# Kernel optimization log

Measured on AMD Instinct MI355X. Metric: run time of the kernel, lower is better.

The kernel has to match this reference:

```python
import jax, jax.numpy as jnp
import numpy as np

B, LQ, LK = 32, 1024, 1024
Q_SIZE, K_SIZE, HID = 1024, 1024, 1024
NEG = -1e9  # masked_softmax fill value for masked positions


def setup_inputs() -> dict:
    key = jax.random.key(0)
    ks = jax.random.split(key, 8)
    scale_q = 1.0 / np.sqrt(Q_SIZE)
    scale_k = 1.0 / np.sqrt(K_SIZE)
    return {
        "query": jax.random.normal(ks[0], (B, LQ, Q_SIZE), dtype=jnp.float32),
        "key": jax.random.normal(ks[1], (B, LK, K_SIZE), dtype=jnp.float32),
        "query_mask": jax.random.randint(ks[2], (B, LQ), 0, 2, dtype=jnp.int32),
        "key_mask": jax.random.randint(ks[3], (B, LK), 0, 2, dtype=jnp.int32),
        "Wq": jax.random.normal(ks[4], (HID, Q_SIZE), dtype=jnp.float32) * scale_q,
        "bq": jnp.zeros((HID,), dtype=jnp.float32),
        "Wk": jax.random.normal(ks[5], (HID, K_SIZE), dtype=jnp.float32) * scale_k,
        "bk": jnp.zeros((HID,), dtype=jnp.float32),
    }


def reference(query, key, query_mask, key_mask, Wq, bq, Wk, bk):
    # FCNet: weight-norm Linear + ReLU (dropout identity at inference)
    q = jax.nn.relu(jnp.einsum("bqd,hd->bqh", query, Wq) + bq)  # [B,LQ,HID]
    k = jax.nn.relu(jnp.einsum("bkd,hd->bkh", key, Wk) + bk)    # [B,LK,HID]
    logits = jnp.einsum("bqh,bkh->bqk", q, k)                   # [B,LQ,LK]
    # masked_softmax over key dim: masked positions -> -inf
    masked = jnp.where(key_mask[:, None, :] != 0, logits, NEG)
    w = jax.nn.softmax(masked, axis=-1)
    # post-softmax query-mask multiply
    w = w * query_mask.astype(w.dtype)[:, :, None]
    return w
```

## Files before the change

### kernel.cpp

```cpp
#include <hip/hip_runtime.h>
#include <stdint.h>

#define B_SZ 32
#define LQ   1024
#define LK   1024
#define HID  1024
#define KDIM 1024

#define LQC  640
#define NT_M 5

#define BM 128
#define BN 128
#define BK 32

typedef __bf16    bf16x8 __attribute__((ext_vector_type(8)));
typedef _Float16  f16x8  __attribute__((ext_vector_type(8)));
typedef float     f32x4  __attribute__((ext_vector_type(4)));

typedef void __attribute__((address_space(1)))* gptr1_t;
typedef void __attribute__((address_space(3)))* lptr3_t;

__device__ __forceinline__ void async_cp16(const void* g, void* l) {
  __builtin_amdgcn_global_load_lds((gptr1_t)g, (lptr3_t)l, 16, 0, 0);
}

__device__ __forceinline__ __bf16 bits_to_bf16(unsigned short s) {
  return __builtin_bit_cast(__bf16, s);
}

__device__ __forceinline__ void split4(const f32x4 x, bf16x8& hi, bf16x8& lo, int base) {
#pragma unroll
  for (int e = 0; e < 4; ++e) {
    float v = x[e];
    unsigned u = __float_as_uint(v);
    float fh = __uint_as_float(u & 0xffff0000u);
    hi[base + e] = bits_to_bf16((unsigned short)(u >> 16));
    lo[base + e] = (__bf16)(v - fh);
  }
}

__global__ __launch_bounds__(256) void mask_scan2(
    const int* __restrict__ qmask, const int* __restrict__ kmask,
    int* __restrict__ qpos, int* __restrict__ kpos,
    int* __restrict__ qidx, int* __restrict__ kidx,
    int* __restrict__ qcnt, int* __restrict__ kcnt) {
  const int which = blockIdx.x >> 5;
  const int b = blockIdx.x & 31;
  const int* mask = which ? kmask : qmask;
  int* pos = which ? kpos : qpos;
  int* idx = which ? kidx : qidx;
  int* cnt = which ? kcnt : qcnt;

  const int tid = threadIdx.x;
  __shared__ int sums[256];
  int4 m4 = ((const int4*)(mask + b * 1024))[tid];
  int m[4] = {m4.x != 0, m4.y != 0, m4.z != 0, m4.w != 0};
  int local = m[0] + m[1] + m[2] + m[3];
  sums[tid] = local;
  __syncthreads();
  for (int off = 1; off < 256; off <<= 1) {
    int v = (tid >= off) ? sums[tid - off] : 0;
    __syncthreads();
    sums[tid] += v;
    __syncthreads();
  }
  int base = sums[tid] - local;
  int total = sums[255];
  if (total > LQC) total = LQC;
  int p = base;
#pragma unroll
  for (int e = 0; e < 4; ++e) {
    pos[b * 1024 + tid * 4 + e] = p;
    if (m[e] && p < LQC) idx[b * LQC + p] = tid * 4 + e;
    p += m[e];
  }
  if (tid == 0) cnt[b] = total;
  __syncthreads();
  for (int q = total + tid; q < LQC; q += 256) idx[b * LQC + q] = 0;
}

__global__ __launch_bounds__(256) void proj_gemm_c(
    const float* __restrict__ query, const float* __restrict__ key,
    const float* __restrict__ Wq, const float* __restrict__ Wk,
    const float* __restrict__ bq, const float* __restrict__ bk,
    const int* __restrict__ qidx, const int* __restrict__ kidx,
    const int* __restrict__ qcnt, const int* __restrict__ kcnt,
    _Float16* __restrict__ qcF, _Float16* __restrict__ kcF) {
  const int inp = blockIdx.y / (B_SZ * NT_M);
  const int rem = blockIdx.y % (B_SZ * NT_M);
  const int b = rem / NT_M, t = rem % NT_M;
  const float* A    = inp ? key  : query;
  const float* W    = inp ? Wk   : Wq;
  const float* bias = inp ? bk   : bq;
  const int*   idx  = inp ? kidx : qidx;
  const int*   cnt  = inp ? kcnt : qcnt;
  _Float16*    outF = inp ? kcF  : qcF;
  if (t * 128 >= cnt[b]) return;

  __shared__ __align__(16) float As[BM * BK];
  __shared__ __align__(16) float Bs[BN * BK];
  const int tid  = threadIdx.x;
  const int wave = tid >> 6, lane = tid & 63;
  const int q    = lane >> 4, l16 = lane & 15;
  const int bn   = blockIdx.x * BN;
  const int wm   = (wave >> 1) * 64, wn = (wave & 1) * 64;

  int arows[4];
#pragma unroll
  for (int i = 0; i < 4; ++i) {
    int rit = (i * 256 + tid) >> 3;
    arows[i] = idx[b * LQC + t * 128 + rit];
  }

  f32x4 acc[4][4] = {};

  for (int k0 = 0; k0 < KDIM; k0 += BK) {
#pragma unroll
    for (int i = 0; i < 4; ++i) {
      int s = i * 256 + tid;
      int row = s >> 3;
      int c = (s & 7) ^ (row & 7);
      async_cp16(A + ((size_t)(b * 1024 + arows[i])) * KDIM + k0 + c * 4, As + s * 4);
      async_cp16(W + (size_t)(bn + row) * KDIM + k0 + c * 4, Bs + s * 4);
    }
    __syncthreads();

    bf16x8 ah[4], al[4], bh[4], bl[4];
#pragma unroll
    for (int t4 = 0; t4 < 4; ++t4) {
      int ra = wm + t4 * 16 + l16;
      int c0 = (q * 2) ^ (ra & 7), c1 = (q * 2 + 1) ^ (ra & 7);
      f32x4 x0 = *(const f32x4*)(As + ra * BK + c0 * 4);
      f32x4 x1 = *(const f32x4*)(As + ra * BK + c1 * 4);
      split4(x0, ah[t4], al[t4], 0);
      split4(x1, ah[t4], al[t4], 4);
      int rb = wn + t4 * 16 + l16;
      int d0 = (q * 2) ^ (rb & 7), d1 = (q * 2 + 1) ^ (rb & 7);
      f32x4 y0 = *(const f32x4*)(Bs + rb * BK + d0 * 4);
      f32x4 y1 = *(const f32x4*)(Bs + rb * BK + d1 * 4);
      split4(y0, bh[t4], bl[t4], 0);
      split4(y1, bh[t4], bl[t4], 4);
    }
#pragma unroll
    for (int i = 0; i < 4; ++i)
#pragma unroll
      for (int j = 0; j < 4; ++j) {
        acc[i][j] = __builtin_amdgcn_mfma_f32_16x16x32_bf16(ah[i], bh[j], acc[i][j], 0, 0, 0);
        acc[i][j] = __builtin_amdgcn_mfma_f32_16x16x32_bf16(ah[i], bl[j], acc[i][j], 0, 0, 0);
        acc[i][j] = __builtin_amdgcn_mfma_f32_16x16x32_bf16(al[i], bh[j], acc[i][j], 0, 0, 0);
      }
    __syncthreads();
  }

#pragma unroll
  for (int j = 0; j < 4; ++j) {
    int n = bn + wn + j * 16 + l16;
    float bv = bias[n];
#pragma unroll
    for (int i = 0; i < 4; ++i) {
#pragma unroll
      for (int r = 0; r < 4; ++r) {
        int mloc = t * 128 + wm + i * 16 + q * 4 + r;
        float v = fmaxf(acc[i][j][r] + bv, 0.0f);
        outF[((size_t)(b * LQC + mloc)) * HID + n] = (_Float16)v;
      }
    }
  }
}

__global__ __launch_bounds__(256) void logits_gemm_f16(
    const _Float16* __restrict__ qF, const _Float16* __restrict__ kF,
    const int* __restrict__ qcnt, const int* __restrict__ kcnt,
    float* __restrict__ Lc) {
  const int b = blockIdx.z;
  const int bm = blockIdx.y * BM, bn = blockIdx.x * BN;
  if (bm >= qcnt[b] || bn >= kcnt[b]) return;

  __shared__ __align__(16) _Float16 As[BM * BK];
  __shared__ __align__(16) _Float16 Bs[BN * BK];
  const int tid  = threadIdx.x;
  const int wave = tid >> 6, lane = tid & 63;
  const int q    = lane >> 4, l16 = lane & 15;
  const int wm   = (wave >> 1) * 64, wn = (wave & 1) * 64;
  const size_t bo = (size_t)b * LQC * HID;

  f32x4 acc[4][4] = {};

  for (int k0 = 0; k0 < HID; k0 += BK) {
#pragma unroll
    for (int i = 0; i < 2; ++i) {
      int s = i * 256 + tid;
      int row = s >> 2;
      int c = (s & 3) ^ ((row ^ (row >> 2)) & 3);
      async_cp16(qF + bo + (size_t)(bm + row) * HID + k0 + c * 8, As + s * 8);
      async_cp16(kF + bo + (size_t)(bn + row) * HID + k0 + c * 8, Bs + s * 8);
    }
    __syncthreads();

    f16x8 ah[4], bh[4];
#pragma unroll
    for (int t = 0; t < 4; ++t) {
      int ra = wm + t * 16 + l16;
      int ca = q ^ ((ra ^ (ra >> 2)) & 3);
      ah[t] = *(const f16x8*)(As + ra * BK + ca * 8);
      int rb = wn + t * 16 + l16;
      int cb = q ^ ((rb ^ (rb >> 2)) & 3);
      bh[t] = *(const f16x8*)(Bs + rb * BK + cb * 8);
    }
#pragma unroll
    for (int i = 0; i < 4; ++i)
#pragma unroll
      for (int j = 0; j < 4; ++j)
        acc[i][j] = __builtin_amdgcn_mfma_f32_16x16x32_f16(ah[i], bh[j], acc[i][j], 0, 0, 0);
    __syncthreads();
  }

  float* o = Lc + (size_t)b * LQC * LQC;
#pragma unroll
  for (int i = 0; i < 4; ++i)
#pragma unroll
    for (int j = 0; j < 4; ++j)
#pragma unroll
      for (int r = 0; r < 4; ++r) {
        int m = bm + wm + i * 16 + q * 4 + r;
        int n = bn + wn + j * 16 + l16;
        o[(size_t)m * LQC + n] = acc[i][j][r];
      }
}

__global__ __launch_bounds__(256) void softmax_scatter_w(
    const float* __restrict__ Lc,
    const int* __restrict__ qmask, const int* __restrict__ qpos,
    const int* __restrict__ kmask, const int* __restrict__ kpos,
    const int* __restrict__ kcnt, float* __restrict__ out) {
  const int tid = threadIdx.x, wave = tid >> 6, lane = tid & 63;
  const int row = blockIdx.x * 4 + wave;
  const int b   = row >> 10;
  float* orow = out + (size_t)row * LK;

  __shared__ float probs[4][LQC];
  const bool active = (qmask[row] != 0);
  float inv = 0.0f;

  if (active) {
    const int kc = kcnt[b];
    const float* g = Lc + ((size_t)b * LQC + qpos[row]) * LQC;
    float v[10];
    float mx = -1e30f;
#pragma unroll
    for (int s = 0; s < 2; ++s) {
      int j = s * 256 + lane * 4;
      f32x4 t = *(const f32x4*)(g + j);
#pragma unroll
      for (int e = 0; e < 4; ++e) {
        float x = (j + e < kc) ? t[e] : -1e9f;
        v[s * 4 + e] = x;
        mx = fmaxf(mx, x);
      }
    }
    {
      int j = 512 + lane * 2;
      float2 t = *(const float2*)(g + j);
      float x0 = (j < kc) ? t.x : -1e9f;
      float x1 = (j + 1 < kc) ? t.y : -1e9f;
      v[8] = x0; v[9] = x1;
      mx = fmaxf(mx, fmaxf(x0, x1));
    }
#pragma unroll
    for (int o = 32; o > 0; o >>= 1) mx = fmaxf(mx, __shfl_xor(mx, o, 64));

    float s_local = 0.0f;
#pragma unroll
    for (int s = 0; s < 2; ++s) {
      int j = s * 256 + lane * 4;
#pragma unroll
      for (int e = 0; e < 4; ++e) {
        float ev = __expf(v[s * 4 + e] - mx);
        probs[wave][j + e] = ev;
        s_local += ev;
      }
    }
    {
      int j = 512 + lane * 2;
      float e0 = __expf(v[8] - mx), e1 = __expf(v[9] - mx);
      probs[wave][j] = e0; probs[wave][j + 1] = e1;
      s_local += e0 + e1;
    }
#pragma unroll
    for (int o = 32; o > 0; o >>= 1) s_local += __shfl_xor(s_local, o, 64);
    inv = 1.0f / s_local;
  }

  __syncthreads();

  const int4* km4p = (const int4*)(kmask + b * LK);
  const int4* kp4p = (const int4*)(kpos + b * LK);
#pragma unroll
  for (int s = 0; s < 4; ++s) {
    int g4 = s * 64 + lane;
    f32x4 o4 = {0.f, 0.f, 0.f, 0.f};
    if (active) {
      int4 km = km4p[g4];
      int4 kp = kp4p[g4];
      const int* kme = (const int*)&km;
      const int* kpe = (const int*)&kp;
#pragma unroll
      for (int e = 0; e < 4; ++e)
        o4[e] = (kme[e] != 0) ? probs[wave][kpe[e]] * inv : 0.0f;
    }
    ((f32x4*)orow)[g4] = o4;
  }
}

extern "C" void kernel_launch(void* const* d_in, const int* in_sizes, int n_in,
                              void* d_out, int out_size, void* d_ws, size_t ws_size,
                              hipStream_t stream) {
  (void)in_sizes; (void)n_in; (void)out_size; (void)ws_size;
  const float* query = (const float*)d_in[0];
  const float* key   = (const float*)d_in[1];
  const int*   qmask = (const int*)d_in[2];
  const int*   kmask = (const int*)d_in[3];
  const float* Wq    = (const float*)d_in[4];
  const float* bq    = (const float*)d_in[5];
  const float* Wk    = (const float*)d_in[6];
  const float* bk    = (const float*)d_in[7];
  float* out = (float*)d_out;

  char* p = (char*)d_ws;
  int* qcnt = (int*)p; p += 128;
  int* kcnt = (int*)p; p += 128;
  int* qidx = (int*)p; p += (size_t)B_SZ * LQC * 4;
  int* kidx = (int*)p; p += (size_t)B_SZ * LQC * 4;
  int* qpos = (int*)p; p += (size_t)B_SZ * LQ * 4;
  int* kpos = (int*)p; p += (size_t)B_SZ * LK * 4;
  _Float16* qcF = (_Float16*)p; p += (size_t)B_SZ * LQC * HID * 2;
  _Float16* kcF = (_Float16*)p; p += (size_t)B_SZ * LQC * HID * 2;
  float* Lc = (float*)p;

  dim3 blk(256);
  mask_scan2<<<dim3(64), blk, 0, stream>>>(qmask, kmask, qpos, kpos, qidx, kidx, qcnt, kcnt);
  proj_gemm_c<<<dim3(HID / BN, 2 * B_SZ * NT_M), blk, 0, stream>>>(
      query, key, Wq, Wk, bq, bk, qidx, kidx, qcnt, kcnt, qcF, kcF);
  logits_gemm_f16<<<dim3(NT_M, NT_M, B_SZ), blk, 0, stream>>>(qcF, kcF, qcnt, kcnt, Lc);
  softmax_scatter_w<<<dim3(B_SZ * LQ / 4), blk, 0, stream>>>(Lc, qmask, qpos, kmask, kpos, kcnt, out);
}
```

Measured before the change: 644.7 us.

## Pre-split fp32 inputs into bf16 hi/lo planes before projection GEMM

Adds a pre-pass that gathers the compacted query/key rows and splits them, along with both weight matrices, into bf16 high and low planes in workspace. A new projection GEMM then loads those planes straight into LDS with async copies and runs three bf16 MFMAs per tile, so the split is no longer recomputed inside the GEMM. The planes reuse the logits buffer region, and the path is only taken when the workspace is large enough. The cost is an extra kernel and extra global traffic to write and re-read the planes, which are larger than the original fp32 rows.

Result: slower. 666.0 us (+3.3%).

```diff
diff --git a/kernel.cpp b/kernel.cpp
--- a/kernel.cpp
+++ b/kernel.cpp
@@ -17,6 +17,7 @@
 typedef __bf16    bf16x8 __attribute__((ext_vector_type(8)));
 typedef _Float16  f16x8  __attribute__((ext_vector_type(8)));
 typedef float     f32x4  __attribute__((ext_vector_type(4)));
+typedef unsigned short u16x8 __attribute__((ext_vector_type(8)));
 
 typedef void __attribute__((address_space(1)))* gptr1_t;
 typedef void __attribute__((address_space(3)))* lptr3_t;
@@ -78,6 +79,144 @@
   if (tid == 0) cnt[b] = total;
   __syncthreads();
   for (int q = total + tid; q < LQC; q += 256) idx[b * LQC + q] = 0;
+}
+
+#define SPLIT_ROWS (2048 + 2 * B_SZ * LQC)
+__global__ __launch_bounds__(256) void split_planes(
+    const float* __restrict__ query, const float* __restrict__ key,
+    const float* __restrict__ Wq, const float* __restrict__ Wk,
+    const int* __restrict__ qidx, const int* __restrict__ kidx,
+    unsigned short* __restrict__ WqH, unsigned short* __restrict__ WqL,
+    unsigned short* __restrict__ WkH, unsigned short* __restrict__ WkL,
+    unsigned short* __restrict__ qH, unsigned short* __restrict__ qL,
+    unsigned short* __restrict__ kH, unsigned short* __restrict__ kL) {
+  const int rowid = blockIdx.x * 2 + (threadIdx.x >> 7);
+  const int t = threadIdx.x & 127;
+  const float* src;
+  unsigned short *dh, *dl;
+  if (rowid < 2048) {
+    const int w = rowid >> 10, r = rowid & 1023;
+    src = (w ? Wk : Wq) + (size_t)r * KDIM;
+    dh = (w ? WkH : WqH) + (size_t)r * KDIM;
+    dl = (w ? WkL : WqL) + (size_t)r * KDIM;
+  } else {
+    int r = rowid - 2048;
+    const int w = (r >= B_SZ * LQC);
+    if (w) r -= B_SZ * LQC;
+    const int b = r / LQC, i = r - b * LQC;
+    const int sr = (w ? kidx : qidx)[b * LQC + i];
+    src = (w ? key : query) + ((size_t)(b * 1024 + sr)) * KDIM;
+    dh = (w ? kH : qH) + ((size_t)(b * LQC + i)) * KDIM;
+    dl = (w ? kL : qL) + ((size_t)(b * LQC + i)) * KDIM;
+  }
+  f32x4 v0 = ((const f32x4*)src)[t * 2];
+  f32x4 v1 = ((const f32x4*)src)[t * 2 + 1];
+  u16x8 h, l;
+#pragma unroll
+  for (int e = 0; e < 4; ++e) {
+    {
+      unsigned u = __float_as_uint(v0[e]);
+      h[e] = (unsigned short)(u >> 16);
+      float fh = __uint_as_float(u & 0xffff0000u);
+      l[e] = __builtin_bit_cast(unsigned short, (__bf16)(v0[e] - fh));
+    }
+    {
+      unsigned u = __float_as_uint(v1[e]);
+      h[4 + e] = (unsigned short)(u >> 16);
+      float fh = __uint_as_float(u & 0xffff0000u);
+      l[4 + e] = __builtin_bit_cast(unsigned short, (__bf16)(v1[e] - fh));
+    }
+  }
+  ((u16x8*)dh)[t] = h;
+  ((u16x8*)dl)[t] = l;
+}
+
+__global__ __launch_bounds__(256) void proj_gemm_c2(
+    const unsigned short* __restrict__ qH, const unsigned short* __restrict__ qL,
+    const unsigned short* __restrict__ kH, const unsigned short* __restrict__ kL,
+    const unsigned short* __restrict__ WqH, const unsigned short* __restrict__ WqL,
+    const unsigned short* __restrict__ WkH, const unsigned short* __restrict__ WkL,
+    const float* __restrict__ bq, const float* __restrict__ bk,
+    const int* __restrict__ qcnt, const int* __restrict__ kcnt,
+    _Float16* __restrict__ qcF, _Float16* __restrict__ kcF) {
+  const int inp = blockIdx.y / (B_SZ * NT_M);
+  const int rem = blockIdx.y % (B_SZ * NT_M);
+  const int b = rem / NT_M, t = rem % NT_M;
+  const unsigned short* AH = inp ? kH : qH;
+  const unsigned short* AL = inp ? kL : qL;
+  const unsigned short* BH = inp ? WkH : WqH;
+  const unsigned short* BL = inp ? WkL : WqL;
+  const float* bias = inp ? bk : bq;
+  const int* cnt = inp ? kcnt : qcnt;
+  _Float16* outF = inp ? kcF : qcF;
+  if (t * 128 >= cnt[b]) return;
+
+  __shared__ __align__(16) unsigned short AsH[BM * BK];
+  __shared__ __align__(16) unsigned short AsL[BM * BK];
+  __shared__ __align__(16) unsigned short BsH[BN * BK];
+  __shared__ __align__(16) unsigned short BsL[BN * BK];
+  const int tid = threadIdx.x;
+  const int wave = tid >> 6, lane = tid & 63;
+  const int q = lane >> 4, l16 = lane & 15;
+  const int bn = blockIdx.x * BN;
+  const int wm = (wave >> 1) * 64, wn = (wave & 1) * 64;
+
+  const size_t abase = ((size_t)(b * LQC + t * 128)) * KDIM;
+  const size_t bbase = (size_t)bn * KDIM;
+
+  f32x4 acc[4][4] = {};
+
+  for (int k0 = 0; k0 < KDIM; k0 += BK) {
+#pragma unroll
+    for (int i = 0; i < 2; ++i) {
+      int s = i * 256 + tid;
+      int row = s >> 2;
+      int c = (s & 3) ^ ((row ^ (row >> 2)) & 3);
+      size_t go = (size_t)row * KDIM + k0 + c * 8;
+      async_cp16(AH + abase + go, AsH + s * 8);
+      async_cp16(AL + abase + go, AsL + s * 8);
+      async_cp16(BH + bbase + go, BsH + s * 8);
+      async_cp16(BL + bbase + go, BsL + s * 8);
+    }
+    __syncthreads();
+
+    bf16x8 ah[4], al[4], bh[4], bl[4];
+#pragma unroll
+    for (int t4 = 0; t4 < 4; ++t4) {
+      int ra = wm + t4 * 16 + l16;
+      int ca = q ^ ((ra ^ (ra >> 2)) & 3);
+      ah[t4] = *(const bf16x8*)(const void*)(AsH + ra * BK + ca * 8);
+      al[t4] = *(const bf16x8*)(const void*)(AsL + ra * BK + ca * 8);
+      int rb = wn + t4 * 16 + l16;
+      int cb = q ^ ((rb ^ (rb >> 2)) & 3);
+      bh[t4] = *(const bf16x8*)(const void*)(BsH + rb * BK + cb * 8);
+      bl[t4] = *(const bf16x8*)(const void*)(BsL + rb * BK + cb * 8);
+    }
+#pragma unroll
+    for (int i = 0; i < 4; ++i)
+#pragma unroll
+      for (int j = 0; j < 4; ++j) {
+        acc[i][j] = __builtin_amdgcn_mfma_f32_16x16x32_bf16(ah[i], bh[j], acc[i][j], 0, 0, 0);
+        acc[i][j] = __builtin_amdgcn_mfma_f32_16x16x32_bf16(ah[i], bl[j], acc[i][j], 0, 0, 0);
+        acc[i][j] = __builtin_amdgcn_mfma_f32_16x16x32_bf16(al[i], bh[j], acc[i][j], 0, 0, 0);
+      }
+    __syncthreads();
+  }
+
+#pragma unroll
+  for (int j = 0; j < 4; ++j) {
+    int n = bn + wn + j * 16 + l16;
+    float bv = bias[n];
+#pragma unroll
+    for (int i = 0; i < 4; ++i) {
+#pragma unroll
+      for (int r = 0; r < 4; ++r) {
+        int mloc = t * 128 + wm + i * 16 + q * 4 + r;
+        float v = fmaxf(acc[i][j][r] + bv, 0.0f);
+        outF[((size_t)(b * LQC + mloc)) * HID + n] = (_Float16)v;
+      }
+    }
+  }
 }
 
 __global__ __launch_bounds__(256) void proj_gemm_c(
@@ -316,7 +455,7 @@
 extern "C" void kernel_launch(void* const* d_in, const int* in_sizes, int n_in,
                               void* d_out, int out_size, void* d_ws, size_t ws_size,
                               hipStream_t stream) {
-  (void)in_sizes; (void)n_in; (void)out_size; (void)ws_size;
+  (void)in_sizes; (void)n_in; (void)out_size;
   const float* query = (const float*)d_in[0];
   const float* key   = (const float*)d_in[1];
   const int*   qmask = (const int*)d_in[2];
@@ -336,12 +475,36 @@
   int* kpos = (int*)p; p += (size_t)B_SZ * LK * 4;
   _Float16* qcF = (_Float16*)p; p += (size_t)B_SZ * LQC * HID * 2;
   _Float16* kcF = (_Float16*)p; p += (size_t)B_SZ * LQC * HID * 2;
-  float* Lc = (float*)p;
+
+  char* u = p;
+  unsigned short* WqH = (unsigned short*)u;
+  unsigned short* WqL = WqH + (size_t)HID * KDIM;
+  unsigned short* WkH = WqL + (size_t)HID * KDIM;
+  unsigned short* WkL = WkH + (size_t)HID * KDIM;
+  unsigned short* qH  = WkL + (size_t)HID * KDIM;
+  unsigned short* qL  = qH + (size_t)B_SZ * LQC * KDIM;
+  unsigned short* kH  = qL + (size_t)B_SZ * LQC * KDIM;
+  unsigned short* kL  = kH + (size_t)B_SZ * LQC * KDIM;
+  float* Lc = (float*)u;
+
+  const size_t planes_bytes = (4 * (size_t)HID * KDIM + 4 * (size_t)B_SZ * LQC * KDIM) * 2;
+  const size_t lc_bytes = (size_t)B_SZ * LQC * LQC * 4;
+  const size_t fixed = (size_t)(p - (char*)d_ws);
+  const size_t need = fixed + (planes_bytes > lc_bytes ? planes_bytes : lc_bytes);
 
   dim3 blk(256);
   mask_scan2<<<dim3(64), blk, 0, stream>>>(qmask, kmask, qpos, kpos, qidx, kidx, qcnt, kcnt);
-  proj_gemm_c<<<dim3(HID / BN, 2 * B_SZ * NT_M), blk, 0, stream>>>(
-      query, key, Wq, Wk, bq, bk, qidx, kidx, qcnt, kcnt, qcF, kcF);
+
+  if (ws_size >= need) {
+    split_planes<<<dim3(SPLIT_ROWS / 2), blk, 0, stream>>>(
+        query, key, Wq, Wk, qidx, kidx, WqH, WqL, WkH, WkL, qH, qL, kH, kL);
+    proj_gemm_c2<<<dim3(HID / BN, 2 * B_SZ * NT_M), blk, 0, stream>>>(
+        qH, qL, kH, kL, WqH, WqL, WkH, WkL, bq, bk, qcnt, kcnt, qcF, kcF);
+  } else {
+    proj_gemm_c<<<dim3(HID / BN, 2 * B_SZ * NT_M), blk, 0, stream>>>(
+        query, key, Wq, Wk, bq, bk, qidx, kidx, qcnt, kcnt, qcF, kcF);
+  }
+
   logits_gemm_f16<<<dim3(NT_M, NT_M, B_SZ), blk, 0, stream>>>(qcF, kcF, qcnt, kcnt, Lc);
   softmax_scatter_w<<<dim3(B_SZ * LQ / 4), blk, 0, stream>>>(Lc, qmask, qpos, kmask, kpos, kcnt, out);
 }
```
